# Optimization experiments

Measured on AMD Instinct MI355X. Metric: run time of the kernel, lower is better.

The kernel has to match this reference:

```python
import jax, jax.numpy as jnp
import numpy as np

WS = 7            # window_size
HEADS = 3
HEAD_DIM = 32
DISP = WS // 2    # displacement = 3
SCALE = HEAD_DIM ** -0.5
NEG = float('-inf')

def _create_mask(upper_lower, left_right):
    m = np.zeros((WS * WS, WS * WS), dtype=np.float32)
    if upper_lower:
        m[-DISP * WS:, :-DISP * WS] = NEG
        m[:-DISP * WS, -DISP * WS:] = NEG
    if left_right:
        m = m.reshape(WS, WS, WS, WS)
        m[:, -DISP:, :, :-DISP] = NEG
        m[:, :-DISP, :, -DISP:] = NEG
        m = m.reshape(WS * WS, WS * WS)
    return m

_UL = jnp.asarray(_create_mask(True, False))   # upper/lower boundary mask [49,49]
_LR = jnp.asarray(_create_mask(False, True))   # left/right boundary mask  [49,49]
_idx = np.array([[i, j] for i in range(WS) for j in range(WS)])
_REL = _idx[None, :, :] - _idx[:, None, :] + WS - 1  # static relative indices [49,49,2]


def setup_inputs() -> dict:
    key = jax.random.key(0)
    ks = jax.random.split(key, 10)
    dim = 96
    inner = HEADS * HEAD_DIM  # 96
    mid = dim                 # dim // 16 = 6 < 10 -> middle_channel = dim per CA code
    B, H, W = 8, 224, 224
    s = lambda k, shape: jax.random.normal(k, shape, jnp.float32) * 0.02
    return {
        "x": jax.random.normal(ks[0], (B, H, W, dim), jnp.float32),
        "w_qkv": s(ks[1], (dim, inner * 3)),
        "pos_emb": jax.random.normal(ks[2], (2 * WS - 1, 2 * WS - 1), jnp.float32),
        "w_out": s(ks[3], (inner, dim)),
        "b_out": jnp.zeros((dim,), jnp.float32),
        "mlp1_w1": s(ks[4], (dim, mid)), "mlp1_b1": jnp.zeros((mid,), jnp.float32),
        "mlp1_w2": s(ks[5], (mid, dim)), "mlp1_b2": jnp.zeros((dim,), jnp.float32),
        "mlp2_w1": s(ks[6], (dim, mid)), "mlp2_b1": jnp.zeros((mid,), jnp.float32),
        "mlp2_w2": s(ks[7], (mid, dim)), "mlp2_b2": jnp.zeros((dim,), jnp.float32),
    }


def reference(x, w_qkv, pos_emb, w_out, b_out,
              mlp1_w1, mlp1_b1, mlp1_w2, mlp1_b2,
              mlp2_w1, mlp2_b1, mlp2_w2, mlp2_b2):
    B, H, W, C = x.shape
    nw_h, nw_w = H // WS, W // WS
    # cyclic shift
    xs = jnp.roll(x, (-DISP, -DISP), axis=(1, 2))
    # qkv projection (no bias)
    q, k, v = jnp.split(xs @ w_qkv, 3, axis=-1)

    def to_win(t):  # [B,H,W,inner] -> [B,heads,n_windows,49,head_dim]
        t = t.reshape(B, nw_h, WS, nw_w, WS, HEADS, HEAD_DIM)
        return t.transpose(0, 5, 1, 3, 2, 4, 6).reshape(B, HEADS, nw_h * nw_w, WS * WS, HEAD_DIM)

    q, k, v = to_win(q), to_win(k), to_win(v)
    dots = jnp.einsum('bhwid,bhwjd->bhwij', q, k) * SCALE
    dots = dots + pos_emb[_REL[..., 0], _REL[..., 1]]  # relative position bias [49,49]
    # boundary window masks for shifted attention
    dots = dots.at[:, :, -nw_w:].add(_UL)
    dots = dots.at[:, :, nw_w - 1::nw_w].add(_LR)
    attn = jax.nn.softmax(dots, axis=-1)
    out = jnp.einsum('bhwij,bhwjd->bhwid', attn, v)
    out = out.reshape(B, HEADS, nw_h, nw_w, WS, WS, HEAD_DIM)
    out = out.transpose(0, 2, 4, 3, 5, 1, 6).reshape(B, H, W, HEADS * HEAD_DIM)
    out = out @ w_out + b_out
    out = jnp.roll(out, (DISP, DISP), axis=(1, 2))  # cyclic back-shift
    # CA channel attention: avg/max pool over spatial -> two MLPs -> sigmoid gate
    avg = out.mean(axis=(1, 2))                     # [B,C]
    mx = out.max(axis=(1, 2))                       # [B,C]
    a = jax.nn.relu(avg @ mlp1_w1 + mlp1_b1) @ mlp1_w2 + mlp1_b2
    m = jax.nn.relu(mx @ mlp2_w1 + mlp2_b1) @ mlp2_w2 + mlp2_b2
    gate = jax.nn.sigmoid(a + m)
    return out * gate[:, None, None, :]
```

## Files before the change

kernel.cpp:

```cpp
#include <hip/hip_runtime.h>
#include <hip/hip_bf16.h>

typedef __attribute__((ext_vector_type(8))) __bf16 bf16x8;
typedef __attribute__((ext_vector_type(4))) float f32x4;
typedef unsigned short u16;
typedef unsigned long long u64;

#define SCALE_QK 0.17677669529663687f

static __device__ __forceinline__ u16 f2b(float f) {
    union { __bf16 h; u16 u; } z; z.h = (__bf16)f; return z.u;
}
static __device__ __forceinline__ float bu2f(u16 s) {
    union { unsigned u; float f; } z; z.u = ((unsigned)s) << 16; return z.f;
}
static __device__ __forceinline__ f32x4 mfma16(bf16x8 a, bf16x8 b, f32x4 c) {
    return __builtin_amdgcn_mfma_f32_16x16x32_bf16(a, b, c, 0, 0, 0);
}
static __device__ __forceinline__ bf16x8 ldfrag(const u16* p) {
    return *(const bf16x8*)p;
}
static __device__ __forceinline__ u64 pack4(float a, float b, float c, float d) {
    union { __bf16 h[4]; u64 q; } z;
    z.h[0] = (__bf16)a; z.h[1] = (__bf16)b; z.h[2] = (__bf16)c; z.h[3] = (__bf16)d;
    return z.q;
}
static __device__ __forceinline__ bf16x8 pack8(float4 a, float4 b) {
    union { __bf16 h[8]; bf16x8 v; } z;
    z.h[0] = (__bf16)a.x; z.h[1] = (__bf16)a.y; z.h[2] = (__bf16)a.z; z.h[3] = (__bf16)a.w;
    z.h[4] = (__bf16)b.x; z.h[5] = (__bf16)b.y; z.h[6] = (__bf16)b.z; z.h[7] = (__bf16)b.w;
    return z.v;
}

__global__ __launch_bounds__(256) void prep_weights(
    const float* __restrict__ w_qkv, const float* __restrict__ w_out,
    u16* __restrict__ wsq, u16* __restrict__ wso)
{
    int idx = blockIdx.x * 256 + threadIdx.x;
    if (idx < 27648) {
        int e = idx & 7, lA = (idx >> 3) & 63;
        int rest = idx >> 9;
        int ks = rest % 3, sec = (rest / 3) % 6, h = rest / 18;
        int krow = ks * 32 + (lA >> 4) * 8 + e;
        int n = lA & 15;
        int gcol;
        if (sec < 2)      gcol = h * 32 + sec * 16 + n;
        else if (sec < 4) gcol = 96 + h * 32 + (sec - 2) * 16 + n;
        else              gcol = 192 + h * 32 + (sec - 4) * 16 + n;
        wsq[idx] = f2b(w_qkv[krow * 288 + gcol]);
    }
    if (idx < 9216) {
        int e = idx & 7, lA = (idx >> 3) & 63;
        int rest = idx >> 9;
        int nt = rest % 6, h = rest / 6;
        int krow = h * 32 + (lA >> 4) * 8 + e;
        wso[idx] = f2b(w_out[krow * 96 + nt * 16 + (lA & 15)]);
    }
}

__global__ __launch_bounds__(256, 4) void swin_attn_mfma(
    const float* __restrict__ x,
    const float* __restrict__ pos_emb,
    const u16*  __restrict__ wsq,
    const u16*  __restrict__ wso,
    const float* __restrict__ b_out,
    float* __restrict__ outf,
    u16*  __restrict__ outw,
    float* __restrict__ psum_win,
    float* __restrict__ pmax_win,
    int write_bf16)
{
    __shared__ __attribute__((aligned(16))) u16 qo_s[64 * 40];
    __shared__ __attribute__((aligned(16))) u16 k_s[64 * 40];
    __shared__ __attribute__((aligned(16))) u16 p_s[64 * 72];
    __shared__ __attribute__((aligned(16))) u16 vT_s[32 * 72];
    __shared__ float rsum[4 * 96];
    __shared__ float rmax[4 * 96];

    const int blk = blockIdx.x;
    const int b = blk >> 10, win = blk & 1023;
    const int wh = win >> 5, ww = win & 31;
    const int tid = threadIdx.x;
    const int w = tid >> 6, l = tid & 63, lr = l & 15, lg = l >> 4;
    const int myrow = 16 * w + lr;

    bf16x8 ax0, ax1, ax2;
    {
        int sr = wh * 7 + myrow / 7 + 3;  if (sr >= 224) sr -= 224;
        int sc = ww * 7 + myrow % 7 + 3;  if (sc >= 224) sc -= 224;
        const float* xr = x + (((size_t)b * 224 + sr) * 224 + sc) * 96 + lg * 8;
        ax0 = pack8(*(const float4*)(xr +  0), *(const float4*)(xr +  4));
        ax1 = pack8(*(const float4*)(xr + 32), *(const float4*)(xr + 36));
        ax2 = pack8(*(const float4*)(xr + 64), *(const float4*)(xr + 68));
    }

    float bias[4][4];
    {
        const bool mUL = (wh == 31), mLR = (ww == 31);
        const int i = myrow;
        const int ir = i / 7, ic = i - ir * 7;
        #pragma unroll
        for (int jt = 0; jt < 4; ++jt) {
            #pragma unroll
            for (int reg = 0; reg < 4; ++reg) {
                int j = jt * 16 + lg * 4 + reg;
                float v;
                if (j >= 49) v = -1e30f;
                else if (i >= 49) v = 0.f;
                else {
                    int jr = j / 7, jc = j - jr * 7;
                    v = pos_emb[(jr - ir + 6) * 13 + (jc - ic + 6)];
                    if (mUL && ((ir >= 4) != (jr >= 4))) v = -1e30f;
                    if (mLR && ((ic >= 4) != (jc >= 4))) v = -1e30f;
                }
                bias[jt][reg] = v;
            }
        }
    }

    f32x4 proj[6];
    #pragma unroll
    for (int nt = 0; nt < 6; ++nt) proj[nt] = (f32x4){0.f, 0.f, 0.f, 0.f};

    for (int h = 0; h < 3; ++h) {
        if (h) __syncthreads();

        #pragma unroll
        for (int sec = 0; sec < 6; ++sec) {
            const u16* wb = wsq + ((size_t)(h * 6 + sec) * 3 * 64 + l) * 8;
            f32x4 c = {0.f, 0.f, 0.f, 0.f};
            if (sec < 4) {
                c = mfma16(ldfrag(wb), ax0, c);
                c = mfma16(ldfrag(wb + 512), ax1, c);
                c = mfma16(ldfrag(wb + 1024), ax2, c);
                u64 pk = pack4(c[0], c[1], c[2], c[3]);
                if (sec < 2)
                    *(u64*)&qo_s[myrow * 40 + (sec & 1) * 16 + lg * 4] = pk;
                else
                    *(u64*)&k_s[myrow * 40 + (sec & 1) * 16 + lg * 4] = pk;
            } else {
                c = mfma16(ax0, ldfrag(wb), c);
                c = mfma16(ax1, ldfrag(wb + 512), c);
                c = mfma16(ax2, ldfrag(wb + 1024), c);
                u64 pk = pack4(c[0], c[1], c[2], c[3]);
                *(u64*)&vT_s[((sec - 4) * 16 + lr) * 72 + 16 * w + lg * 4] = pk;
            }
        }
        __syncthreads();

        bf16x8 bq = ldfrag(&qo_s[myrow * 40 + lg * 8]);
        f32x4 S[4];
        #pragma unroll
        for (int jt = 0; jt < 4; ++jt) {
            f32x4 z = {0.f, 0.f, 0.f, 0.f};
            S[jt] = mfma16(ldfrag(&k_s[(jt * 16 + lr) * 40 + lg * 8]), bq, z);
        }

        float ssum = 0.f;
        float e[4][4];
        #pragma unroll
        for (int jt = 0; jt < 4; ++jt) {
            #pragma unroll
            for (int reg = 0; reg < 4; ++reg) {
                float v = __expf(fmaf(S[jt][reg], SCALE_QK, bias[jt][reg]));
                e[jt][reg] = v; ssum += v;
            }
        }
        ssum += __shfl_xor(ssum, 16);
        ssum += __shfl_xor(ssum, 32);
        float inv = 1.f / ssum;
        #pragma unroll
        for (int jt = 0; jt < 4; ++jt)
            *(u64*)&p_s[myrow * 72 + jt * 16 + lg * 4] =
                pack4(e[jt][0], e[jt][1], e[jt][2], e[jt][3]);

        bf16x8 bp0 = ldfrag(&p_s[myrow * 72 +  0 + lg * 8]);
        bf16x8 bp1 = ldfrag(&p_s[myrow * 72 + 32 + lg * 8]);
        #pragma unroll
        for (int mt = 0; mt < 2; ++mt) {
            f32x4 c = {0.f, 0.f, 0.f, 0.f};
            c = mfma16(ldfrag(&vT_s[(mt * 16 + lr) * 72 +  0 + lg * 8]), bp0, c);
            c = mfma16(ldfrag(&vT_s[(mt * 16 + lr) * 72 + 32 + lg * 8]), bp1, c);
            *(u64*)&qo_s[myrow * 40 + mt * 16 + lg * 4] =
                pack4(c[0] * inv, c[1] * inv, c[2] * inv, c[3] * inv);
        }

        bf16x8 ao = ldfrag(&qo_s[myrow * 40 + lg * 8]);
        #pragma unroll
        for (int nt = 0; nt < 6; ++nt) {
            const u16* wb = wso + ((size_t)(h * 6 + nt) * 64 + l) * 8;
            proj[nt] = mfma16(ao, ldfrag(wb), proj[nt]);
        }
    }

    float csum[6], cmax[6];
    #pragma unroll
    for (int nt = 0; nt < 6; ++nt) { csum[nt] = 0.f; cmax[nt] = -1e30f; }
    #pragma unroll
    for (int nt = 0; nt < 6; ++nt) {
        int c = nt * 16 + lr;
        float bo = b_out[c];
        #pragma unroll
        for (int reg = 0; reg < 4; ++reg) {
            int tok = 16 * w + lg * 4 + reg;
            if (tok < 49) {
                float v = proj[nt][reg] + bo;
                int sr = wh * 7 + tok / 7 + 3;  if (sr >= 224) sr -= 224;
                int sc = ww * 7 + tok % 7 + 3;  if (sc >= 224) sc -= 224;
                size_t o = (((size_t)b * 224 + sr) * 224 + sc) * 96 + c;
                if (write_bf16) outw[o] = f2b(v);
                else            outf[o] = v;
                csum[nt] += v;
                cmax[nt] = fmaxf(cmax[nt], v);
            }
        }
    }
    #pragma unroll
    for (int nt = 0; nt < 6; ++nt) {
        csum[nt] += __shfl_xor(csum[nt], 16);
        csum[nt] += __shfl_xor(csum[nt], 32);
        cmax[nt] = fmaxf(cmax[nt], __shfl_xor(cmax[nt], 16));
        cmax[nt] = fmaxf(cmax[nt], __shfl_xor(cmax[nt], 32));
    }
    if (lg == 0) {
        #pragma unroll
        for (int nt = 0; nt < 6; ++nt) {
            rsum[w * 96 + nt * 16 + lr] = csum[nt];
            rmax[w * 96 + nt * 16 + lr] = cmax[nt];
        }
    }
    __syncthreads();
    if (tid < 96) {
        size_t o = ((size_t)b * 1024 + win) * 96 + tid;
        psum_win[o] = rsum[tid] + rsum[96 + tid] + rsum[192 + tid] + rsum[288 + tid];
        pmax_win[o] = fmaxf(fmaxf(rmax[tid], rmax[96 + tid]),
                            fmaxf(rmax[192 + tid], rmax[288 + tid]));
    }
}

__global__ __launch_bounds__(384) void gate_kernel(
    const float* __restrict__ psum, const float* __restrict__ pmax,
    const float* __restrict__ w11, const float* __restrict__ b11,
    const float* __restrict__ w12, const float* __restrict__ b12,
    const float* __restrict__ w21, const float* __restrict__ b21,
    const float* __restrict__ w22, const float* __restrict__ b22,
    float* __restrict__ gate)
{
    const int b = blockIdx.x;
    const int tid = threadIdx.x;
    const int c = tid % 96, sub = tid / 96;
    __shared__ float ls[384], lm[384];
    __shared__ float avg[96], mx[96], h1[96], h2[96];

    float s = 0.f, m = -1e30f;
    for (int k = sub * 256; k < sub * 256 + 256; ++k) {
        size_t o = ((size_t)b * 1024 + k) * 96 + c;
        s += psum[o];
        m = fmaxf(m, pmax[o]);
    }
    ls[tid] = s; lm[tid] = m;
    __syncthreads();
    if (tid < 96) {
        s = ls[c] + ls[96 + c] + ls[192 + c] + ls[288 + c];
        m = fmaxf(fmaxf(lm[c], lm[96 + c]), fmaxf(lm[192 + c], lm[288 + c]));
        avg[c] = s * (1.0f / 50176.0f);
        mx[c]  = m;
    }
    __syncthreads();
    if (tid < 96) {
        float sa = b11[c], sm = b21[c];
        for (int ic = 0; ic < 96; ++ic) {
            sa = fmaf(avg[ic], w11[ic * 96 + c], sa);
            sm = fmaf(mx[ic],  w21[ic * 96 + c], sm);
        }
        h1[c] = fmaxf(sa, 0.f);
        h2[c] = fmaxf(sm, 0.f);
    }
    __syncthreads();
    if (tid < 96) {
        float a = b12[c], m2 = b22[c];
        for (int hh = 0; hh < 96; ++hh) {
            a  = fmaf(h1[hh], w12[hh * 96 + c], a);
            m2 = fmaf(h2[hh], w22[hh * 96 + c], m2);
        }
        float g = a + m2;
        gate[b * 96 + c] = 1.0f / (1.0f + __expf(-g));
    }
}

__global__ __launch_bounds__(256) void scale_bf16_kernel(
    const u16* __restrict__ outw, float* __restrict__ out,
    const float* __restrict__ gate)
{
    const size_t total8 = 38535168u / 8;
    for (size_t i8 = (size_t)blockIdx.x * blockDim.x + threadIdx.x; i8 < total8;
         i8 += (size_t)gridDim.x * blockDim.x) {
        size_t base = i8 * 8;
        int c = (int)(base % 96);
        int b = (int)(base / ((size_t)50176 * 96));
        u64 pk0 = *(const u64*)(outw + base);
        u64 pk1 = *(const u64*)(outw + base + 4);
        float4 g0 = *(const float4*)(gate + b * 96 + c);
        float4 g1 = *(const float4*)(gate + b * 96 + c + 4);
        float4 o0, o1;
        o0.x = bu2f((u16)(pk0      )) * g0.x;
        o0.y = bu2f((u16)(pk0 >> 16)) * g0.y;
        o0.z = bu2f((u16)(pk0 >> 32)) * g0.z;
        o0.w = bu2f((u16)(pk0 >> 48)) * g0.w;
        o1.x = bu2f((u16)(pk1      )) * g1.x;
        o1.y = bu2f((u16)(pk1 >> 16)) * g1.y;
        o1.z = bu2f((u16)(pk1 >> 32)) * g1.z;
        o1.w = bu2f((u16)(pk1 >> 48)) * g1.w;
        *(float4*)(out + base)     = o0;
        *(float4*)(out + base + 4) = o1;
    }
}

__global__ __launch_bounds__(256) void scale_f32_kernel(
    float* __restrict__ out, const float* __restrict__ gate)
{
    const size_t total4 = 38535168u / 4;
    for (size_t i4 = (size_t)blockIdx.x * blockDim.x + threadIdx.x; i4 < total4;
         i4 += (size_t)gridDim.x * blockDim.x) {
        size_t base = i4 * 4;
        int c = (int)(base % 96);
        int b = (int)(base / ((size_t)50176 * 96));
        float4 u = ((const float4*)out)[i4];
        float4 g = *(const float4*)(gate + b * 96 + c);
        float4 o;
        o.x = u.x * g.x; o.y = u.y * g.y; o.z = u.z * g.z; o.w = u.w * g.w;
        ((float4*)out)[i4] = o;
    }
}

extern "C" void kernel_launch(void* const* d_in, const int* in_sizes, int n_in,
                              void* d_out, int out_size, void* d_ws, size_t ws_size,
                              hipStream_t stream) {
    const float* x     = (const float*)d_in[0];
    const float* wqkv  = (const float*)d_in[1];
    const float* pos   = (const float*)d_in[2];
    const float* wout  = (const float*)d_in[3];
    const float* bout  = (const float*)d_in[4];
    const float* m1w1  = (const float*)d_in[5];
    const float* m1b1  = (const float*)d_in[6];
    const float* m1w2  = (const float*)d_in[7];
    const float* m1b2  = (const float*)d_in[8];
    const float* m2w1  = (const float*)d_in[9];
    const float* m2b1  = (const float*)d_in[10];
    const float* m2w2  = (const float*)d_in[11];
    const float* m2b2  = (const float*)d_in[12];
    float* out = (float*)d_out;

    float* psum_win = (float*)d_ws;
    float* pmax_win = psum_win + 8 * 1024 * 96;
    float* gatep    = pmax_win + 8 * 1024 * 96;
    u16*   wsq      = (u16*)(gatep + 8 * 96);
    u16*   wso      = wsq + 27648;
    u16*   outw     = wso + 9216;

    const size_t base_bytes = (size_t)((char*)outw - (char*)d_ws);
    const size_t outw_bytes = (size_t)8 * 50176 * 96 * sizeof(u16);
    const int use_bf16 = (ws_size >= base_bytes + outw_bytes) ? 1 : 0;

    hipLaunchKernelGGL(prep_weights, dim3(108), dim3(256), 0, stream,
                       wqkv, wout, wsq, wso);
    hipLaunchKernelGGL(swin_attn_mfma, dim3(8192), dim3(256), 0, stream,
                       x, pos, wsq, wso, bout,
                       use_bf16 ? nullptr : out, use_bf16 ? outw : nullptr,
                       psum_win, pmax_win, use_bf16);
    hipLaunchKernelGGL(gate_kernel, dim3(8), dim3(384), 0, stream,
                       psum_win, pmax_win, m1w1, m1b1, m1w2, m1b2,
                       m2w1, m2b1, m2w2, m2b2, gatep);
    if (use_bf16) {
        hipLaunchKernelGGL(scale_bf16_kernel, dim3(2048), dim3(256), 0, stream,
                           outw, out, gatep);
    } else {
        hipLaunchKernelGGL(scale_f32_kernel, dim3(2048), dim3(256), 0, stream,
                           out, gatep);
    }
}
```

Before: 249.6 us.

## Swizzle LDS tiles, merge Q/K buffers, alias reduce scratch, raise occupancy

Replaces the padded LDS layouts (row strides 40/72) with unpadded 64-element rows that use an XOR swizzle on the column index, to avoid bank conflicts. Q and K now share one buffer, and the per-warp reduction scratch reuses the P buffer behind an extra barrier. Together these shrink shared memory per block, and the launch bounds move from 4 to 6 blocks per CU to raise occupancy. The tighter register budget may cause spills, and the added barrier costs a little.

Result: slower. 338.5 us (+35.6%).

```diff
diff --git a/kernel.cpp b/kernel.cpp
--- a/kernel.cpp
+++ b/kernel.cpp
@@ -30,6 +30,12 @@
     z.h[0] = (__bf16)a.x; z.h[1] = (__bf16)a.y; z.h[2] = (__bf16)a.z; z.h[3] = (__bf16)a.w;
     z.h[4] = (__bf16)b.x; z.h[5] = (__bf16)b.y; z.h[6] = (__bf16)b.z; z.h[7] = (__bf16)b.w;
     return z.v;
+}
+static __device__ __forceinline__ void st4(u16* base, int row, int col, u64 v) {
+    *(u64*)&base[(row << 6) + (col ^ ((row & 7) << 3))] = v;
+}
+static __device__ __forceinline__ bf16x8 ld8(const u16* base, int row, int col) {
+    return *(const bf16x8*)&base[(row << 6) + (col ^ ((row & 7) << 3))];
 }
 
 __global__ __launch_bounds__(256) void prep_weights(
@@ -58,7 +64,7 @@
     }
 }
 
-__global__ __launch_bounds__(256, 4) void swin_attn_mfma(
+__global__ __launch_bounds__(256, 6) void swin_attn_mfma(
     const float* __restrict__ x,
     const float* __restrict__ pos_emb,
     const u16*  __restrict__ wsq,
@@ -70,12 +76,9 @@
     float* __restrict__ pmax_win,
     int write_bf16)
 {
-    __shared__ __attribute__((aligned(16))) u16 qo_s[64 * 40];
-    __shared__ __attribute__((aligned(16))) u16 k_s[64 * 40];
-    __shared__ __attribute__((aligned(16))) u16 p_s[64 * 72];
-    __shared__ __attribute__((aligned(16))) u16 vT_s[32 * 72];
-    __shared__ float rsum[4 * 96];
-    __shared__ float rmax[4 * 96];
+    __shared__ __attribute__((aligned(16))) u16 qk_s[64 * 64];
+    __shared__ __attribute__((aligned(16))) u16 p_s[64 * 64];
+    __shared__ __attribute__((aligned(16))) u16 vT_s[32 * 64];
 
     const int blk = blockIdx.x;
     const int b = blk >> 10, win = blk & 1023;
@@ -118,6 +121,9 @@
         }
     }
 
+    const u16* wsq_l = wsq + l * 8;
+    const u16* wso_l = wso + l * 8;
+
     f32x4 proj[6];
     #pragma unroll
     for (int nt = 0; nt < 6; ++nt) proj[nt] = (f32x4){0.f, 0.f, 0.f, 0.f};
@@ -127,33 +133,30 @@
 
         #pragma unroll
         for (int sec = 0; sec < 6; ++sec) {
-            const u16* wb = wsq + ((size_t)(h * 6 + sec) * 3 * 64 + l) * 8;
+            const u16* wb = wsq_l + (size_t)(h * 18 + sec * 3) * 512;
             f32x4 c = {0.f, 0.f, 0.f, 0.f};
             if (sec < 4) {
                 c = mfma16(ldfrag(wb), ax0, c);
                 c = mfma16(ldfrag(wb + 512), ax1, c);
                 c = mfma16(ldfrag(wb + 1024), ax2, c);
                 u64 pk = pack4(c[0], c[1], c[2], c[3]);
-                if (sec < 2)
-                    *(u64*)&qo_s[myrow * 40 + (sec & 1) * 16 + lg * 4] = pk;
-                else
-                    *(u64*)&k_s[myrow * 40 + (sec & 1) * 16 + lg * 4] = pk;
+                st4(qk_s, myrow, (sec < 2 ? 0 : 32) + (sec & 1) * 16 + lg * 4, pk);
             } else {
                 c = mfma16(ax0, ldfrag(wb), c);
                 c = mfma16(ax1, ldfrag(wb + 512), c);
                 c = mfma16(ax2, ldfrag(wb + 1024), c);
                 u64 pk = pack4(c[0], c[1], c[2], c[3]);
-                *(u64*)&vT_s[((sec - 4) * 16 + lr) * 72 + 16 * w + lg * 4] = pk;
+                st4(vT_s, (sec - 4) * 16 + lr, 16 * w + lg * 4, pk);
             }
         }
         __syncthreads();
 
-        bf16x8 bq = ldfrag(&qo_s[myrow * 40 + lg * 8]);
+        bf16x8 bq = ld8(qk_s, myrow, lg * 8);
         f32x4 S[4];
         #pragma unroll
         for (int jt = 0; jt < 4; ++jt) {
             f32x4 z = {0.f, 0.f, 0.f, 0.f};
-            S[jt] = mfma16(ldfrag(&k_s[(jt * 16 + lr) * 40 + lg * 8]), bq, z);
+            S[jt] = mfma16(ld8(qk_s, jt * 16 + lr, 32 + lg * 8), bq, z);
         }
 
         float ssum = 0.f;
@@ -171,26 +174,25 @@
         float inv = 1.f / ssum;
         #pragma unroll
         for (int jt = 0; jt < 4; ++jt)
-            *(u64*)&p_s[myrow * 72 + jt * 16 + lg * 4] =
-                pack4(e[jt][0], e[jt][1], e[jt][2], e[jt][3]);
-
-        bf16x8 bp0 = ldfrag(&p_s[myrow * 72 +  0 + lg * 8]);
-        bf16x8 bp1 = ldfrag(&p_s[myrow * 72 + 32 + lg * 8]);
+            st4(p_s, myrow, jt * 16 + lg * 4,
+                pack4(e[jt][0], e[jt][1], e[jt][2], e[jt][3]));
+
+        bf16x8 bp0 = ld8(p_s, myrow, lg * 8);
+        bf16x8 bp1 = ld8(p_s, myrow, 32 + lg * 8);
         #pragma unroll
         for (int mt = 0; mt < 2; ++mt) {
             f32x4 c = {0.f, 0.f, 0.f, 0.f};
-            c = mfma16(ldfrag(&vT_s[(mt * 16 + lr) * 72 +  0 + lg * 8]), bp0, c);
-            c = mfma16(ldfrag(&vT_s[(mt * 16 + lr) * 72 + 32 + lg * 8]), bp1, c);
-            *(u64*)&qo_s[myrow * 40 + mt * 16 + lg * 4] =
-                pack4(c[0] * inv, c[1] * inv, c[2] * inv, c[3] * inv);
-        }
-
-        bf16x8 ao = ldfrag(&qo_s[myrow * 40 + lg * 8]);
-        #pragma unroll
-        for (int nt = 0; nt < 6; ++nt) {
-            const u16* wb = wso + ((size_t)(h * 6 + nt) * 64 + l) * 8;
-            proj[nt] = mfma16(ao, ldfrag(wb), proj[nt]);
-        }
+            c = mfma16(ld8(vT_s, mt * 16 + lr,  0 + lg * 8), bp0, c);
+            c = mfma16(ld8(vT_s, mt * 16 + lr, 32 + lg * 8), bp1, c);
+            st4(qk_s, myrow, mt * 16 + lg * 4,
+                pack4(c[0] * inv, c[1] * inv, c[2] * inv, c[3] * inv));
+        }
+
+        bf16x8 ao = ld8(qk_s, myrow, lg * 8);
+        #pragma unroll
+        for (int nt = 0; nt < 6; ++nt)
+            proj[nt] = mfma16(ao, ldfrag(wso_l + (size_t)(h * 6 + nt) * 512),
+                              proj[nt]);
     }
 
     float csum[6], cmax[6];
@@ -222,6 +224,9 @@
         cmax[nt] = fmaxf(cmax[nt], __shfl_xor(cmax[nt], 16));
         cmax[nt] = fmaxf(cmax[nt], __shfl_xor(cmax[nt], 32));
     }
+    float* rsum = (float*)p_s;
+    float* rmax = rsum + 384;
+    __syncthreads();
     if (lg == 0) {
         #pragma unroll
         for (int nt = 0; nt < 6; ++nt) {
```
